# Kernel optimization log

Hardware: AMD Instinct MI355X
Metric: run time of the kernel (lower is better)

## Reference

```python
import jax, jax.numpy as jnp
import numpy as np

B, L, D, H, FF, V, NL = 1024, 200, 128, 4, 512, 100001, 2
DK = D // H
EPS = 1e-5


def layer_norm(x, w, b):
    mu = jnp.mean(x, axis=-1, keepdims=True)
    var = jnp.mean(jnp.square(x - mu), axis=-1, keepdims=True)
    return (x - mu) * jax.lax.rsqrt(var + EPS) * w + b


def setup_inputs() -> dict:
    key = jax.random.key(0)
    ks = jax.random.split(key, 32)
    s = 0.02
    d = {}
    d["batch_seqs"] = jax.random.randint(ks[0], (B, L), 0, V, dtype=jnp.int32)
    d["token_emb"] = jax.random.normal(ks[1], (V, D), jnp.float32) * s
    d["pos_emb"] = jax.random.normal(ks[2], (L, D), jnp.float32) * s
    # per-layer stacked params, leading axis = layer
    d["Wq"] = jax.random.normal(ks[3], (NL, D, D), jnp.float32) * s
    d["bq"] = jnp.zeros((NL, D), jnp.float32)
    d["Wk"] = jax.random.normal(ks[4], (NL, D, D), jnp.float32) * s
    d["bk"] = jnp.zeros((NL, D), jnp.float32)
    d["Wv"] = jax.random.normal(ks[5], (NL, D, D), jnp.float32) * s
    d["bv"] = jnp.zeros((NL, D), jnp.float32)
    d["Wo"] = jax.random.normal(ks[6], (NL, D, D), jnp.float32) * s
    d["bo"] = jnp.zeros((NL, D), jnp.float32)
    d["ln1_w"] = jnp.ones((NL, D), jnp.float32)
    d["ln1_b"] = jnp.zeros((NL, D), jnp.float32)
    d["ln2_w"] = jnp.ones((NL, D), jnp.float32)
    d["ln2_b"] = jnp.zeros((NL, D), jnp.float32)
    d["W1"] = jax.random.normal(ks[7], (NL, D, FF), jnp.float32) * s
    d["b1"] = jnp.zeros((NL, FF), jnp.float32)
    d["W2"] = jax.random.normal(ks[8], (NL, FF, D), jnp.float32) * s
    d["b2"] = jnp.zeros((NL, D), jnp.float32)
    d["fc_W"] = jax.random.normal(ks[9], (L * D, D), jnp.float32) * s
    d["fc_b"] = jnp.zeros((D,), jnp.float32)
    return d


def reference(batch_seqs, token_emb, pos_emb, Wq, bq, Wk, bk, Wv, bv, Wo, bo,
              ln1_w, ln1_b, ln2_w, ln2_b, W1, b1, W2, b2, fc_W, fc_b):
    # key-padding mask: [B,1,1,L] (broadcasts over heads and queries)
    mask = (batch_seqs > 0)[:, None, None, :]
    x = token_emb[batch_seqs] + pos_emb[None, :, :]  # [B,L,D]
    scale = 1.0 / jnp.sqrt(jnp.float32(DK))
    for i in range(NL):
        h = layer_norm(x, ln1_w[i], ln1_b[i])
        q = (h @ Wq[i] + bq[i]).reshape(B, L, H, DK)
        k = (h @ Wk[i] + bk[i]).reshape(B, L, H, DK)
        v = (h @ Wv[i] + bv[i]).reshape(B, L, H, DK)
        scores = jnp.einsum('bqhd,bkhd->bhqk', q, k) * scale
        scores = jnp.where(mask, scores, -1e9)
        p = jax.nn.softmax(scores, axis=-1)
        attn = jnp.einsum('bhqk,bkhd->bqhd', p, v).reshape(B, L, D)
        x = x + (attn @ Wo[i] + bo[i])
        h = layer_norm(x, ln2_w[i], ln2_b[i])
        ffn = jax.nn.gelu(h @ W1[i] + b1[i], approximate=False) @ W2[i] + b2[i]
        x = x + ffn
    # FlattenLayers: flatten [B, L*D] -> Linear -> [B, D]
    out = x.reshape(B, L * D) @ fc_W + fc_b
    return out
```

## Files before the change

### kernel.cpp

```cpp
#include <hip/hip_runtime.h>
#include <math.h>

typedef unsigned short u16;
typedef unsigned int u32;
typedef __attribute__((ext_vector_type(8))) short bf16x8;
typedef __attribute__((ext_vector_type(4))) float f32x4;

#define Bx 1024
#define Lx 200
#define Dx 128
#define FFx 512
#define Mx (Bx*Lx)
#define PVP 232
#define TSP 40

__device__ __forceinline__ u16 f2bf(float f) {
  u32 u = __float_as_uint(f);
  u32 r = (u + 0x7fffu + ((u >> 16) & 1u)) >> 16;
  return (u16)r;
}

__device__ __forceinline__ float gelu_f(float v) {
  float z = v * fmaf(v * v, 0.0713548163f, 1.5957691216f);
  float e = __expf(-z);
  return v * __builtin_amdgcn_rcpf(1.0f + e);
}

union BFCV { u32 u[4]; bf16x8 h; };

struct CvtJobs {
  const float* src[13];
  u16* dst[13];
  int N[13];
  int ks[13];
  int bstart[14];
};

__global__ void k_cvt_all(CvtJobs J) {
  const int b = blockIdx.x;
  int j = 0;
  #pragma unroll 1
  while (b >= J.bstart[j + 1]) ++j;
  const float* __restrict__ src = J.src[j];
  u16* __restrict__ dst = J.dst[j];
  const int N = J.N[j], k_steps = J.ks[j];
  int id = (b - J.bstart[j]) * 256 + threadIdx.x;
  int lane = id & 63;
  int rest = id >> 6;
  int kst = rest % k_steps;
  int ntile = rest / k_steps;
  int n = ntile * 16 + (lane & 15);
  int kb = kst * 32 + ((lane >> 4) << 3);
  const float* sp = src + (size_t)kb * N + n;
  u32 w[4];
  #pragma unroll
  for (int jj = 0; jj < 4; ++jj) {
    u32 lo = f2bf(sp[(size_t)(2 * jj) * N]);
    u32 hi = f2bf(sp[(size_t)(2 * jj + 1) * N]);
    w[jj] = lo | (hi << 16);
  }
  ((uint4*)dst)[id] = make_uint4(w[0], w[1], w[2], w[3]);
}

__global__ void k_embed(const int* __restrict__ seq, const float* __restrict__ tok,
                        const float* __restrict__ pos, float* __restrict__ x) {
  const int i = blockIdx.x * 256 + threadIdx.x;
  const int row = i >> 5, c = i & 31;
  const int t = seq[row];
  const int l = row % Lx;
  const float4 a = ((const float4*)tok)[(size_t)t * 32 + c];
  const float4 p = ((const float4*)pos)[l * 32 + c];
  ((float4*)x)[i] = make_float4(a.x + p.x, a.y + p.y, a.z + p.z, a.w + p.w);
}

__device__ __forceinline__ void reg_ln(const float* __restrict__ xr,
                                       const float* __restrict__ ln_w,
                                       const float* __restrict__ ln_b,
                                       int quad, bf16x8 af[4]) {
  float v[32];
  float s = 0.f, sq = 0.f;
  #pragma unroll
  for (int kst = 0; kst < 4; ++kst) {
    float4 a = *(const float4*)(xr + kst * 32);
    float4 b = *(const float4*)(xr + kst * 32 + 4);
    v[kst * 8 + 0] = a.x; v[kst * 8 + 1] = a.y; v[kst * 8 + 2] = a.z; v[kst * 8 + 3] = a.w;
    v[kst * 8 + 4] = b.x; v[kst * 8 + 5] = b.y; v[kst * 8 + 6] = b.z; v[kst * 8 + 7] = b.w;
  }
  #pragma unroll
  for (int i = 0; i < 32; ++i) { s += v[i]; sq = fmaf(v[i], v[i], sq); }
  s  += __shfl_xor(s, 16);  s  += __shfl_xor(s, 32);
  sq += __shfl_xor(sq, 16); sq += __shfl_xor(sq, 32);
  float mu = s * 0.0078125f;
  float rr = rsqrtf(fmaf(-mu, mu, sq * 0.0078125f) + 1e-5f);
  #pragma unroll
  for (int kst = 0; kst < 4; ++kst) {
    const float* lwp = ln_w + kst * 32 + quad * 8;
    const float* lbp = ln_b + kst * 32 + quad * 8;
    float4 lw0 = *(const float4*)(lwp);
    float4 lw1 = *(const float4*)(lwp + 4);
    float4 lb0 = *(const float4*)(lbp);
    float4 lb1 = *(const float4*)(lbp + 4);
    float hw[8] = {lw0.x, lw0.y, lw0.z, lw0.w, lw1.x, lw1.y, lw1.z, lw1.w};
    float hb[8] = {lb0.x, lb0.y, lb0.z, lb0.w, lb1.x, lb1.y, lb1.z, lb1.w};
    BFCV cv;
    #pragma unroll
    for (int j = 0; j < 4; ++j) {
      float h0 = fmaf((v[kst * 8 + 2 * j]     - mu) * rr, hw[2 * j],     hb[2 * j]);
      float h1 = fmaf((v[kst * 8 + 2 * j + 1] - mu) * rr, hw[2 * j + 1], hb[2 * j + 1]);
      cv.u[j] = (u32)f2bf(h0) | ((u32)f2bf(h1) << 16);
    }
    af[kst] = cv.h;
  }
}

__global__ __launch_bounds__(256, 4)
void k_qkv(const float* __restrict__ x, const float* __restrict__ ln_w,
           const float* __restrict__ ln_b, const u16* __restrict__ Wqkvs,
           const float* __restrict__ bq, const float* __restrict__ bk,
           const float* __restrict__ bv,
           u16* __restrict__ qo, u16* __restrict__ ko, u16* __restrict__ vo) {
  const int tid = threadIdx.x;
  const int row0 = blockIdx.x * 64;
  const int lane = tid & 63, wv = tid >> 6;
  const int l15 = lane & 15, quad = lane >> 4;
  const int m0 = wv * 16;

  bf16x8 af[4];
  reg_ln(x + (size_t)(row0 + m0 + l15) * Dx + quad * 8, ln_w, ln_b, quad, af);

  int bl[4], ll[4];
  #pragma unroll
  for (int r = 0; r < 4; ++r) {
    int gr = row0 + m0 + quad * 4 + r;
    bl[r] = gr / 200;
    ll[r] = gr - bl[r] * 200;
  }

  const float scale = 0.17677669529663687f;
  #pragma unroll
  for (int nt = 0; nt < 24; ++nt) {
    f32x4 acc = (f32x4){0.f, 0.f, 0.f, 0.f};
    const u16* wb = Wqkvs + ((size_t)(nt * 4) * 64 + lane) * 8;
    #pragma unroll
    for (int kst = 0; kst < 4; ++kst) {
      bf16x8 bfr = *(const bf16x8*)(wb + kst * 64 * 8);
      acc = __builtin_amdgcn_mfma_f32_16x16x32_bf16(af[kst], bfr, acc, 0, 0, 0);
    }
    const int col = (nt & 7) * 16 + l15;
    const int head = col >> 5, dk = col & 31;
    if (nt < 8) {
      float bb = bq[col];
      #pragma unroll
      for (int r = 0; r < 4; ++r)
        qo[((size_t)(bl[r] * 4 + head) * 200 + ll[r]) * 32 + dk] = f2bf((acc[r] + bb) * scale);
    } else if (nt < 16) {
      float bb = bk[col];
      #pragma unroll
      for (int r = 0; r < 4; ++r)
        ko[((size_t)(bl[r] * 4 + head) * 200 + ll[r]) * 32 + dk] = f2bf(acc[r] + bb);
    } else {
      float bb = bv[col];
      #pragma unroll
      for (int r = 0; r < 4; ++r)
        vo[((size_t)(bl[r] * 4 + head) * 200 + ll[r]) * 32 + dk] = f2bf(acc[r] + bb);
    }
  }
}

__global__ __launch_bounds__(256, 3)
void k_attn2(const u16* __restrict__ q, const u16* __restrict__ k,
             const u16* __restrict__ v, const int* __restrict__ seq,
             u16* __restrict__ attn) {
  __shared__ float smask[224];
  __shared__ __align__(16) u16 vt[32 * PVP];
  __shared__ __align__(16) u16 Pb[4][16 * PVP];
  const int tid = threadIdx.x;
  const int bl = blockIdx.x >> 2, head = blockIdx.x & 3;
  const int bh = blockIdx.x;
  const int lane = tid & 63, wv = tid >> 6;
  const int l15 = lane & 15, quad = lane >> 4;

  if (tid < 224)
    smask[tid] = (tid < 200 && seq[bl * 200 + tid] > 0) ? 0.f : -1e9f;
  #pragma unroll 1
  for (int e = tid; e < 800; e += 256) {
    int l = e >> 2, g = (e & 3) * 8;
    uint4 pv = *(const uint4*)(v + ((size_t)bh * 200 + l) * 32 + g);
    const u16* pw = (const u16*)&pv;
    #pragma unroll
    for (int j = 0; j < 8; ++j) vt[(g + j) * PVP + l] = pw[j];
  }
  #pragma unroll 1
  for (int e = tid; e < 1024; e += 256) {
    int rr = e >> 5, cc = 200 + (e & 31);
    vt[rr * PVP + cc] = 0;
  }
  __syncthreads();

  float msk[14];
  #pragma unroll
  for (int nt = 0; nt < 14; ++nt) msk[nt] = smask[nt * 16 + l15];

  const u16* qbase = q + (size_t)bh * 200 * 32;
  const u16* kbase = k + (size_t)bh * 200 * 32;
  u16* Pw = Pb[wv];

  #pragma unroll 1
  for (int mt = wv; mt < 13; mt += 4) {
    bf16x8 qf = *(const bf16x8*)(qbase + (mt * 16 + l15) * 32 + quad * 8);
    f32x4 s[14];
    #pragma unroll
    for (int nt = 0; nt < 14; ++nt) {
      bf16x8 kf = *(const bf16x8*)(kbase + (nt * 16 + l15) * 32 + quad * 8);
      s[nt] = __builtin_amdgcn_mfma_f32_16x16x32_bf16(qf, kf, (f32x4){0.f, 0.f, 0.f, 0.f}, 0, 0, 0);
    }
    float rmax[4] = {-1e30f, -1e30f, -1e30f, -1e30f};
    #pragma unroll
    for (int nt = 0; nt < 14; ++nt) {
      #pragma unroll
      for (int r = 0; r < 4; ++r) {
        s[nt][r] += msk[nt];
        rmax[r] = fmaxf(rmax[r], s[nt][r]);
      }
    }
    #pragma unroll
    for (int m = 1; m < 16; m <<= 1) {
      #pragma unroll
      for (int r = 0; r < 4; ++r) rmax[r] = fmaxf(rmax[r], __shfl_xor(rmax[r], m));
    }
    float rsum[4] = {0.f, 0.f, 0.f, 0.f};
    #pragma unroll
    for (int nt = 0; nt < 14; ++nt) {
      #pragma unroll
      for (int r = 0; r < 4; ++r) {
        float p = __expf(s[nt][r] - rmax[r]);
        s[nt][r] = p;
        rsum[r] += p;
      }
    }
    #pragma unroll
    for (int m = 1; m < 16; m <<= 1) {
      #pragma unroll
      for (int r = 0; r < 4; ++r) rsum[r] += __shfl_xor(rsum[r], m);
    }
    float inv[4];
    #pragma unroll
    for (int r = 0; r < 4; ++r) inv[r] = 1.0f / rsum[r];
    #pragma unroll
    for (int nt = 0; nt < 14; ++nt) {
      #pragma unroll
      for (int r = 0; r < 4; ++r)
        Pw[(quad * 4 + r) * PVP + nt * 16 + l15] = f2bf(s[nt][r]);
    }
    __asm__ __volatile__("s_waitcnt lgkmcnt(0)" ::: "memory");
    f32x4 o0 = (f32x4){0.f, 0.f, 0.f, 0.f}, o1 = (f32x4){0.f, 0.f, 0.f, 0.f};
    #pragma unroll
    for (int kst = 0; kst < 7; ++kst) {
      bf16x8 pf  = *(const bf16x8*)&Pw[l15 * PVP + kst * 32 + quad * 8];
      bf16x8 vf0 = *(const bf16x8*)&vt[l15 * PVP + kst * 32 + quad * 8];
      bf16x8 vf1 = *(const bf16x8*)&vt[(16 + l15) * PVP + kst * 32 + quad * 8];
      o0 = __builtin_amdgcn_mfma_f32_16x16x32_bf16(pf, vf0, o0, 0, 0, 0);
      o1 = __builtin_amdgcn_mfma_f32_16x16x32_bf16(pf, vf1, o1, 0, 0, 0);
    }
    #pragma unroll
    for (int r = 0; r < 4; ++r) {
      int row = mt * 16 + quad * 4 + r;
      if (row < 200) {
        u16* op = attn + ((size_t)bl * 200 + row) * 128 + head * 32;
        op[l15]      = f2bf(o0[r] * inv[r]);
        op[16 + l15] = f2bf(o1[r] * inv[r]);
      }
    }
  }
}

__global__ __launch_bounds__(256, 4)
void k_oproj(const u16* __restrict__ a, const u16* __restrict__ Wos,
             const float* __restrict__ bo, float* __restrict__ x) {
  const int tid = threadIdx.x;
  const int lane = tid & 63, wv = tid >> 6;
  const int l15 = lane & 15, quad = lane >> 4;
  const size_t m0 = (size_t)blockIdx.x * 64 + wv * 16;
  f32x4 acc[8];
  #pragma unroll
  for (int i = 0; i < 8; ++i) acc[i] = (f32x4){0.f, 0.f, 0.f, 0.f};
  #pragma unroll
  for (int kst = 0; kst < 4; ++kst) {
    bf16x8 af = *(const bf16x8*)(a + (m0 + l15) * Dx + kst * 32 + quad * 8);
    const u16* wb = Wos + (kst * 64 + lane) * 8;
    #pragma unroll
    for (int nt = 0; nt < 8; ++nt) {
      bf16x8 bf = *(const bf16x8*)(wb + nt * (4 * 64 * 8));
      acc[nt] = __builtin_amdgcn_mfma_f32_16x16x32_bf16(af, bf, acc[nt], 0, 0, 0);
    }
  }
  #pragma unroll
  for (int nt = 0; nt < 8; ++nt) {
    int col = nt * 16 + l15;
    float bb = bo[col];
    #pragma unroll
    for (int r = 0; r < 4; ++r) {
      size_t idx = (m0 + quad * 4 + r) * Dx + col;
      x[idx] += acc[nt][r] + bb;
    }
  }
}

__global__ __launch_bounds__(256, 4)
void k_ffn(float* __restrict__ x, const float* __restrict__ ln_w,
           const float* __restrict__ ln_b,
           const u16* __restrict__ W1s, const float* __restrict__ b1,
           const u16* __restrict__ W2s, const float* __restrict__ b2) {
  __shared__ __align__(16) u16 smem[2560 + 8192 + 8192];
  u16* ts  = smem;
  u16* w1b = smem + 2560;
  u16* w2b = smem + 10752;
  const int tid = threadIdx.x;
  const size_t row0 = (size_t)blockIdx.x * 64;
  const int lane = tid & 63, wv = tid >> 6;
  const int l15 = lane & 15, quad = lane >> 4;
  const int m0 = wv * 16;
  const int nt0 = tid >> 6, off = tid & 63;

  bf16x8 af[4];
  reg_ln(x + (row0 + m0 + l15) * (size_t)Dx + quad * 8, ln_w, ln_b, quad, af);

  ((uint4*)w1b)[tid]       = ((const uint4*)(W1s + (size_t)(nt0 * 4) * 512))[off];
  ((uint4*)w1b)[tid + 256] = ((const uint4*)(W1s + (size_t)((nt0 + 4) * 4) * 512))[off];
  ((uint4*)w2b)[tid]       = ((const uint4*)(W2s + (size_t)(nt0 * 16) * 512))[off];
  ((uint4*)w2b)[tid + 256] = ((const uint4*)(W2s + (size_t)((nt0 + 4) * 16) * 512))[off];
  __syncthreads();

  f32x4 acc2[8];
  #pragma unroll
  for (int i = 0; i < 8; ++i) acc2[i] = (f32x4){0.f, 0.f, 0.f, 0.f};

  #pragma unroll 1
  for (int ch = 0; ch < 4; ++ch) {
    f32x4 acc1[8];
    #pragma unroll
    for (int i = 0; i < 8; ++i) acc1[i] = (f32x4){0.f, 0.f, 0.f, 0.f};
    #pragma unroll
    for (int kst = 0; kst < 4; ++kst) {
      uint4 s0, s1;
      if (kst < 3) {
        s0 = ((const uint4*)(W1s + (size_t)((ch * 8 + nt0) * 4 + kst + 1) * 512))[off];
        s1 = ((const uint4*)(W1s + (size_t)((ch * 8 + nt0 + 4) * 4 + kst + 1) * 512))[off];
      }
      const u16* wb = w1b + (kst & 1) * 4096;
      #pragma unroll
      for (int nt = 0; nt < 8; ++nt) {
        bf16x8 bfr = *(const bf16x8*)&wb[nt * 512 + lane * 8];
        acc1[nt] = __builtin_amdgcn_mfma_f32_16x16x32_bf16(af[kst], bfr, acc1[nt], 0, 0, 0);
      }
      if (kst < 3) {
        uint4* d = (uint4*)(w1b + ((kst + 1) & 1) * 4096);
        d[tid] = s0; d[tid + 256] = s1;
      }
      __syncthreads();
    }
    #pragma unroll
    for (int p = 0; p < 4; ++p) {
      uint4 s0, s1, t0, t1;
      const bool s2  = (p < 3);
      const bool s1n = (p == 3) && (ch < 3);
      if (s2) {
        s0 = ((const uint4*)(W2s + (size_t)(nt0 * 16 + ch * 4 + p + 1) * 512))[off];
        s1 = ((const uint4*)(W2s + (size_t)((nt0 + 4) * 16 + ch * 4 + p + 1) * 512))[off];
      }
      if (s1n) {
        s0 = ((const uint4*)(W1s + (size_t)(((ch + 1) * 8 + nt0) * 4) * 512))[off];
        s1 = ((const uint4*)(W1s + (size_t)(((ch + 1) * 8 + nt0 + 4) * 4) * 512))[off];
        t0 = ((const uint4*)(W2s + (size_t)(nt0 * 16 + (ch + 1) * 4) * 512))[off];
        t1 = ((const uint4*)(W2s + (size_t)((nt0 + 4) * 16 + (ch + 1) * 4) * 512))[off];
      }
      #pragma unroll
      for (int q2 = 0; q2 < 2; ++q2) {
        const int ntg = 2 * p + q2;
        float bb = b1[ch * 128 + ntg * 16 + l15];
        #pragma unroll
        for (int r = 0; r < 4; ++r)
          ts[(m0 + quad * 4 + r) * TSP + q2 * 16 + l15] =
              f2bf(gelu_f(acc1[ntg][r] + bb));
      }
      __asm__ __volatile__("s_waitcnt lgkmcnt(0)" ::: "memory");
      bf16x8 tf = *(const bf16x8*)&ts[(m0 + l15) * TSP + quad * 8];
      const u16* wb = w2b + (p & 1) * 4096;
      #pragma unroll
      for (int nt = 0; nt < 8; ++nt) {
        bf16x8 bfr = *(const bf16x8*)&wb[nt * 512 + lane * 8];
        acc2[nt] = __builtin_amdgcn_mfma_f32_16x16x32_bf16(tf, bfr, acc2[nt], 0, 0, 0);
      }
      if (s2) {
        uint4* d = (uint4*)(w2b + ((p + 1) & 1) * 4096);
        d[tid] = s0; d[tid + 256] = s1;
      }
      if (s1n) {
        ((uint4*)w1b)[tid] = s0; ((uint4*)w1b)[tid + 256] = s1;
        ((uint4*)w2b)[tid] = t0; ((uint4*)w2b)[tid + 256] = t1;
      }
      __syncthreads();
    }
  }
  #pragma unroll
  for (int nt = 0; nt < 8; ++nt) {
    int col = nt * 16 + l15;
    float bb = b2[col];
    #pragma unroll
    for (int r = 0; r < 4; ++r) {
      size_t idx = (row0 + m0 + quad * 4 + r) * Dx + col;
      x[idx] += acc2[nt][r] + bb;
    }
  }
}

__global__ __launch_bounds__(256, 4)
void k_fc(const float* __restrict__ x, const u16* __restrict__ fcWs,
          float* __restrict__ part) {
  const int tid = threadIdx.x;
  const int lane = tid & 63, wv = tid >> 6;
  const int l15 = lane & 15, quad = lane >> 4;
  const int m0 = blockIdx.x * 64 + wv * 16;
  const int ky = blockIdx.y;
  f32x4 acc[8];
  #pragma unroll
  for (int i = 0; i < 8; ++i) acc[i] = (f32x4){0.f, 0.f, 0.f, 0.f};
  const float* xp = x + (size_t)(m0 + l15) * 25600 + quad * 8;
  #pragma unroll 1
  for (int kst = ky * 25; kst < ky * 25 + 25; ++kst) {
    float4 xa = *(const float4*)(xp + kst * 32);
    float4 xb2 = *(const float4*)(xp + kst * 32 + 4);
    bf16x8 af;
    af[0] = (short)f2bf(xa.x);  af[1] = (short)f2bf(xa.y);
    af[2] = (short)f2bf(xa.z);  af[3] = (short)f2bf(xa.w);
    af[4] = (short)f2bf(xb2.x); af[5] = (short)f2bf(xb2.y);
    af[6] = (short)f2bf(xb2.z); af[7] = (short)f2bf(xb2.w);
    const u16* wb = fcWs + ((size_t)kst * 64 + lane) * 8;
    #pragma unroll
    for (int nt = 0; nt < 8; ++nt) {
      bf16x8 bf = *(const bf16x8*)(wb + (size_t)nt * (800 * 64 * 8));
      acc[nt] = __builtin_amdgcn_mfma_f32_16x16x32_bf16(af, bf, acc[nt], 0, 0, 0);
    }
  }
  float* pp = part + (size_t)ky * (Bx * Dx);
  #pragma unroll
  for (int nt = 0; nt < 8; ++nt) {
    #pragma unroll
    for (int r = 0; r < 4; ++r) {
      pp[(size_t)(m0 + quad * 4 + r) * Dx + nt * 16 + l15] = acc[nt][r];
    }
  }
}

__global__ void k_fcred(const float* __restrict__ part, const float* __restrict__ fcb,
                        float* __restrict__ out) {
  int i = blockIdx.x * 256 + threadIdx.x;
  float s = fcb[i & 127];
  #pragma unroll
  for (int k = 0; k < 32; ++k) s += part[(size_t)k * (Bx * Dx) + i];
  out[i] = s;
}

extern "C" void kernel_launch(void* const* d_in, const int* in_sizes, int n_in,
                              void* d_out, int out_size, void* d_ws, size_t ws_size,
                              hipStream_t stream) {
  const int*   seq  = (const int*)d_in[0];
  const float* tok  = (const float*)d_in[1];
  const float* pos  = (const float*)d_in[2];
  const float* Wq   = (const float*)d_in[3];
  const float* bq   = (const float*)d_in[4];
  const float* Wk   = (const float*)d_in[5];
  const float* bk   = (const float*)d_in[6];
  const float* Wv   = (const float*)d_in[7];
  const float* bv   = (const float*)d_in[8];
  const float* Wo   = (const float*)d_in[9];
  const float* bo   = (const float*)d_in[10];
  const float* ln1w = (const float*)d_in[11];
  const float* ln1b = (const float*)d_in[12];
  const float* ln2w = (const float*)d_in[13];
  const float* ln2b = (const float*)d_in[14];
  const float* W1   = (const float*)d_in[15];
  const float* b1   = (const float*)d_in[16];
  const float* W2   = (const float*)d_in[17];
  const float* b2   = (const float*)d_in[18];
  const float* fcW  = (const float*)d_in[19];
  const float* fcb  = (const float*)d_in[20];
  float* out = (float*)d_out;

  char* ws = (char*)d_ws;
  const size_t XB = (size_t)Mx * Dx * 4;
  const size_t WBSZ = 7340032;

  int nc = 4;
  for (int t = 1; t <= 4; t <<= 1) {
    size_t qsz = (size_t)(Bx / t) * 51200;
    if (XB + 4 * qsz + WBSZ <= ws_size) { nc = t; break; }
  }
  const int BC = Bx / nc;
  const size_t qsz = (size_t)BC * 51200;

  float* x    = (float*)ws;
  u16* qb     = (u16*)(ws + XB);
  u16* kb     = (u16*)(ws + XB + qsz);
  u16* vb     = (u16*)(ws + XB + 2 * qsz);
  u16* ab     = (u16*)(ws + XB + 3 * qsz);
  float* part = (float*)(ws + XB);
  char* WB    = ws + XB + 4 * qsz;
  u16* W1s0   = (u16*)(WB);
  u16* W1s1   = (u16*)(WB + 131072);
  u16* W2s0   = (u16*)(WB + 262144);
  u16* W2s1   = (u16*)(WB + 393216);
  u16* Wos0   = (u16*)(WB + 524288);
  u16* Wos1   = (u16*)(WB + 557056);
  u16* Wqkvs0 = (u16*)(WB + 589824);
  u16* Wqkvs1 = (u16*)(WB + 688128);
  u16* fcWs   = (u16*)(WB + 786432);

  CvtJobs J;
  const float* srcs[13] = {W1, W1 + Dx * FFx, W2, W2 + FFx * Dx,
                           Wo, Wo + Dx * Dx,
                           Wq, Wk, Wv,
                           Wq + Dx * Dx, Wk + Dx * Dx, Wv + Dx * Dx,
                           fcW};
  u16* dsts[13] = {W1s0, W1s1, W2s0, W2s1, Wos0, Wos1,
                   Wqkvs0, Wqkvs0 + 16384, Wqkvs0 + 32768,
                   Wqkvs1, Wqkvs1 + 16384, Wqkvs1 + 32768,
                   fcWs};
  const int Ns[13]  = {FFx, FFx, Dx, Dx, Dx, Dx, Dx, Dx, Dx, Dx, Dx, Dx, Dx};
  const int kss[13] = {4, 4, 16, 16, 4, 4, 4, 4, 4, 4, 4, 4, 800};
  const int nblk[13] = {32, 32, 32, 32, 8, 8, 8, 8, 8, 8, 8, 8, 1600};
  int acc = 0;
  for (int j = 0; j < 13; ++j) {
    J.src[j] = srcs[j]; J.dst[j] = dsts[j]; J.N[j] = Ns[j]; J.ks[j] = kss[j];
    J.bstart[j] = acc; acc += nblk[j];
  }
  J.bstart[13] = acc;
  k_cvt_all<<<acc, 256, 0, stream>>>(J);

  k_embed<<<25600, 256, 0, stream>>>(seq, tok, pos, x);
  const int cblk = BC * 200 / 64;
  for (int i = 0; i < 2; ++i) {
    const u16* Wqkvs = (i == 0) ? Wqkvs0 : Wqkvs1;
    const u16* Wos   = (i == 0) ? Wos0 : Wos1;
    for (int c = 0; c < nc; ++c) {
      float* xc = x + (size_t)c * BC * 200 * 128;
      const int* seqc = seq + (size_t)c * BC * 200;
      k_qkv<<<cblk, 256, 0, stream>>>(xc, ln1w + i * Dx, ln1b + i * Dx, Wqkvs,
                                      bq + i * Dx, bk + i * Dx, bv + i * Dx,
                                      qb, kb, vb);
      k_attn2<<<BC * 4, 256, 0, stream>>>(qb, kb, vb, seqc, ab);
      k_oproj<<<cblk, 256, 0, stream>>>(ab, Wos, bo + i * Dx, xc);
    }
    k_ffn<<<3200, 256, 0, stream>>>(x, ln2w + i * Dx, ln2b + i * Dx,
                                    (i == 0) ? W1s0 : W1s1, b1 + i * FFx,
                                    (i == 0) ? W2s0 : W2s1, b2 + i * Dx);
  }
  k_fc<<<dim3(16, 32), 256, 0, stream>>>(x, fcWs, part);
  k_fcred<<<512, 256, 0, stream>>>(part, fcb, out);
}
```

Before: 919.0 us.

## Process two 16-row tiles per wave in QKV and FFN kernels

Each wave in k_qkv and k_ffn now computes two 16-row M tiles, so every loaded weight fragment feeds two MFMAs. The QKV kernel handles 128 rows per block, halving its grid. The FFN kernel drops to 128 threads and replaces its separate W1 and W2 double buffers with one shared ping-pong buffer, cutting LDS use. In exchange, accumulator register pressure doubles and there are fewer waves per block, which may reduce occupancy and latency hiding.

Result: slower. 2.044 ms (+122.4%).

```diff
diff --git a/kernel.cpp b/kernel.cpp
--- a/kernel.cpp
+++ b/kernel.cpp
@@ -120,49 +120,62 @@
            const float* __restrict__ bv,
            u16* __restrict__ qo, u16* __restrict__ ko, u16* __restrict__ vo) {
   const int tid = threadIdx.x;
-  const int row0 = blockIdx.x * 64;
+  const int row0 = blockIdx.x * 128;
   const int lane = tid & 63, wv = tid >> 6;
   const int l15 = lane & 15, quad = lane >> 4;
-  const int m0 = wv * 16;
-
-  bf16x8 af[4];
-  reg_ln(x + (size_t)(row0 + m0 + l15) * Dx + quad * 8, ln_w, ln_b, quad, af);
-
-  int bl[4], ll[4];
-  #pragma unroll
-  for (int r = 0; r < 4; ++r) {
-    int gr = row0 + m0 + quad * 4 + r;
-    bl[r] = gr / 200;
-    ll[r] = gr - bl[r] * 200;
-  }
+  const int m0 = wv * 32;
+
+  bf16x8 af[2][4];
+  #pragma unroll
+  for (int rt = 0; rt < 2; ++rt)
+    reg_ln(x + (size_t)(row0 + m0 + rt * 16 + l15) * Dx + quad * 8,
+           ln_w, ln_b, quad, af[rt]);
+
+  int bl[2][4], ll[2][4];
+  #pragma unroll
+  for (int rt = 0; rt < 2; ++rt)
+    #pragma unroll
+    for (int r = 0; r < 4; ++r) {
+      int gr = row0 + m0 + rt * 16 + quad * 4 + r;
+      bl[rt][r] = gr / 200;
+      ll[rt][r] = gr - bl[rt][r] * 200;
+    }
 
   const float scale = 0.17677669529663687f;
   #pragma unroll
   for (int nt = 0; nt < 24; ++nt) {
-    f32x4 acc = (f32x4){0.f, 0.f, 0.f, 0.f};
+    f32x4 a0 = (f32x4){0.f, 0.f, 0.f, 0.f};
+    f32x4 a1 = (f32x4){0.f, 0.f, 0.f, 0.f};
     const u16* wb = Wqkvs + ((size_t)(nt * 4) * 64 + lane) * 8;
     #pragma unroll
     for (int kst = 0; kst < 4; ++kst) {
       bf16x8 bfr = *(const bf16x8*)(wb + kst * 64 * 8);
-      acc = __builtin_amdgcn_mfma_f32_16x16x32_bf16(af[kst], bfr, acc, 0, 0, 0);
+      a0 = __builtin_amdgcn_mfma_f32_16x16x32_bf16(af[0][kst], bfr, a0, 0, 0, 0);
+      a1 = __builtin_amdgcn_mfma_f32_16x16x32_bf16(af[1][kst], bfr, a1, 0, 0, 0);
     }
     const int col = (nt & 7) * 16 + l15;
     const int head = col >> 5, dk = col & 31;
     if (nt < 8) {
       float bb = bq[col];
       #pragma unroll
-      for (int r = 0; r < 4; ++r)
-        qo[((size_t)(bl[r] * 4 + head) * 200 + ll[r]) * 32 + dk] = f2bf((acc[r] + bb) * scale);
+      for (int r = 0; r < 4; ++r) {
+        qo[((size_t)(bl[0][r] * 4 + head) * 200 + ll[0][r]) * 32 + dk] = f2bf((a0[r] + bb) * scale);
+        qo[((size_t)(bl[1][r] * 4 + head) * 200 + ll[1][r]) * 32 + dk] = f2bf((a1[r] + bb) * scale);
+      }
     } else if (nt < 16) {
       float bb = bk[col];
       #pragma unroll
-      for (int r = 0; r < 4; ++r)
-        ko[((size_t)(bl[r] * 4 + head) * 200 + ll[r]) * 32 + dk] = f2bf(acc[r] + bb);
+      for (int r = 0; r < 4; ++r) {
+        ko[((size_t)(bl[0][r] * 4 + head) * 200 + ll[0][r]) * 32 + dk] = f2bf(a0[r] + bb);
+        ko[((size_t)(bl[1][r] * 4 + head) * 200 + ll[1][r]) * 32 + dk] = f2bf(a1[r] + bb);
+      }
     } else {
       float bb = bv[col];
       #pragma unroll
-      for (int r = 0; r < 4; ++r)
-        vo[((size_t)(bl[r] * 4 + head) * 200 + ll[r]) * 32 + dk] = f2bf(acc[r] + bb);
+      for (int r = 0; r < 4; ++r) {
+        vo[((size_t)(bl[0][r] * 4 + head) * 200 + ll[0][r]) * 32 + dk] = f2bf(a0[r] + bb);
+        vo[((size_t)(bl[1][r] * 4 + head) * 200 + ll[1][r]) * 32 + dk] = f2bf(a1[r] + bb);
+      }
     }
   }
 }
@@ -306,112 +319,134 @@
   }
 }
 
-__global__ __launch_bounds__(256, 4)
+__global__ __launch_bounds__(128, 4)
 void k_ffn(float* __restrict__ x, const float* __restrict__ ln_w,
            const float* __restrict__ ln_b,
            const u16* __restrict__ W1s, const float* __restrict__ b1,
            const u16* __restrict__ W2s, const float* __restrict__ b2) {
-  __shared__ __align__(16) u16 smem[2560 + 8192 + 8192];
-  u16* ts  = smem;
-  u16* w1b = smem + 2560;
-  u16* w2b = smem + 10752;
+  __shared__ __align__(16) u16 smem[2560 + 2 * 4096];
+  u16* ts   = smem;
+  u16* wbuf = smem + 2560;
   const int tid = threadIdx.x;
   const size_t row0 = (size_t)blockIdx.x * 64;
   const int lane = tid & 63, wv = tid >> 6;
   const int l15 = lane & 15, quad = lane >> 4;
-  const int m0 = wv * 16;
-  const int nt0 = tid >> 6, off = tid & 63;
-
-  bf16x8 af[4];
-  reg_ln(x + (row0 + m0 + l15) * (size_t)Dx + quad * 8, ln_w, ln_b, quad, af);
-
-  ((uint4*)w1b)[tid]       = ((const uint4*)(W1s + (size_t)(nt0 * 4) * 512))[off];
-  ((uint4*)w1b)[tid + 256] = ((const uint4*)(W1s + (size_t)((nt0 + 4) * 4) * 512))[off];
-  ((uint4*)w2b)[tid]       = ((const uint4*)(W2s + (size_t)(nt0 * 16) * 512))[off];
-  ((uint4*)w2b)[tid + 256] = ((const uint4*)(W2s + (size_t)((nt0 + 4) * 16) * 512))[off];
+  const int m0 = wv * 32;
+
+  bf16x8 af[2][4];
+  #pragma unroll
+  for (int rt = 0; rt < 2; ++rt)
+    reg_ln(x + (row0 + m0 + rt * 16 + l15) * (size_t)Dx + quad * 8,
+           ln_w, ln_b, quad, af[rt]);
+
+  int snt[4], sof[4];
+  #pragma unroll
+  for (int i = 0; i < 4; ++i) { int e = tid + i * 128; snt[i] = e >> 6; sof[i] = e & 63; }
+
+  #pragma unroll
+  for (int i = 0; i < 4; ++i)
+    ((uint4*)wbuf)[tid + i * 128] =
+        ((const uint4*)(W1s + (size_t)(snt[i] * 4) * 512))[sof[i]];
   __syncthreads();
 
-  f32x4 acc2[8];
-  #pragma unroll
-  for (int i = 0; i < 8; ++i) acc2[i] = (f32x4){0.f, 0.f, 0.f, 0.f};
-
+  f32x4 acc2[2][8];
+  #pragma unroll
+  for (int rt = 0; rt < 2; ++rt)
+    #pragma unroll
+    for (int i = 0; i < 8; ++i) acc2[rt][i] = (f32x4){0.f, 0.f, 0.f, 0.f};
+
+  int pq = 0;
   #pragma unroll 1
   for (int ch = 0; ch < 4; ++ch) {
-    f32x4 acc1[8];
-    #pragma unroll
-    for (int i = 0; i < 8; ++i) acc1[i] = (f32x4){0.f, 0.f, 0.f, 0.f};
+    f32x4 acc1[2][8];
+    #pragma unroll
+    for (int rt = 0; rt < 2; ++rt)
+      #pragma unroll
+      for (int i = 0; i < 8; ++i) acc1[rt][i] = (f32x4){0.f, 0.f, 0.f, 0.f};
     #pragma unroll
     for (int kst = 0; kst < 4; ++kst) {
-      uint4 s0, s1;
+      uint4 sg[4];
       if (kst < 3) {
-        s0 = ((const uint4*)(W1s + (size_t)((ch * 8 + nt0) * 4 + kst + 1) * 512))[off];
-        s1 = ((const uint4*)(W1s + (size_t)((ch * 8 + nt0 + 4) * 4 + kst + 1) * 512))[off];
-      }
-      const u16* wb = w1b + (kst & 1) * 4096;
+        #pragma unroll
+        for (int i = 0; i < 4; ++i)
+          sg[i] = ((const uint4*)(W1s + (size_t)((ch * 8 + snt[i]) * 4 + kst + 1) * 512))[sof[i]];
+      } else {
+        #pragma unroll
+        for (int i = 0; i < 4; ++i)
+          sg[i] = ((const uint4*)(W2s + (size_t)(snt[i] * 16 + ch * 4) * 512))[sof[i]];
+      }
+      const u16* wb = wbuf + pq * 4096;
       #pragma unroll
       for (int nt = 0; nt < 8; ++nt) {
         bf16x8 bfr = *(const bf16x8*)&wb[nt * 512 + lane * 8];
-        acc1[nt] = __builtin_amdgcn_mfma_f32_16x16x32_bf16(af[kst], bfr, acc1[nt], 0, 0, 0);
-      }
-      if (kst < 3) {
-        uint4* d = (uint4*)(w1b + ((kst + 1) & 1) * 4096);
-        d[tid] = s0; d[tid + 256] = s1;
+        acc1[0][nt] = __builtin_amdgcn_mfma_f32_16x16x32_bf16(af[0][kst], bfr, acc1[0][nt], 0, 0, 0);
+        acc1[1][nt] = __builtin_amdgcn_mfma_f32_16x16x32_bf16(af[1][kst], bfr, acc1[1][nt], 0, 0, 0);
+      }
+      {
+        uint4* d = (uint4*)(wbuf + (pq ^ 1) * 4096);
+        #pragma unroll
+        for (int i = 0; i < 4; ++i) d[tid + i * 128] = sg[i];
       }
       __syncthreads();
+      pq ^= 1;
     }
     #pragma unroll
     for (int p = 0; p < 4; ++p) {
-      uint4 s0, s1, t0, t1;
-      const bool s2  = (p < 3);
-      const bool s1n = (p == 3) && (ch < 3);
-      if (s2) {
-        s0 = ((const uint4*)(W2s + (size_t)(nt0 * 16 + ch * 4 + p + 1) * 512))[off];
-        s1 = ((const uint4*)(W2s + (size_t)((nt0 + 4) * 16 + ch * 4 + p + 1) * 512))[off];
-      }
-      if (s1n) {
-        s0 = ((const uint4*)(W1s + (size_t)(((ch + 1) * 8 + nt0) * 4) * 512))[off];
-        s1 = ((const uint4*)(W1s + (size_t)(((ch + 1) * 8 + nt0 + 4) * 4) * 512))[off];
-        t0 = ((const uint4*)(W2s + (size_t)(nt0 * 16 + (ch + 1) * 4) * 512))[off];
-        t1 = ((const uint4*)(W2s + (size_t)((nt0 + 4) * 16 + (ch + 1) * 4) * 512))[off];
-      }
-      #pragma unroll
-      for (int q2 = 0; q2 < 2; ++q2) {
-        const int ntg = 2 * p + q2;
-        float bb = b1[ch * 128 + ntg * 16 + l15];
-        #pragma unroll
-        for (int r = 0; r < 4; ++r)
-          ts[(m0 + quad * 4 + r) * TSP + q2 * 16 + l15] =
-              f2bf(gelu_f(acc1[ntg][r] + bb));
-      }
+      uint4 sg[4];
+      bool have = true;
+      if (p < 3) {
+        #pragma unroll
+        for (int i = 0; i < 4; ++i)
+          sg[i] = ((const uint4*)(W2s + (size_t)(snt[i] * 16 + ch * 4 + p + 1) * 512))[sof[i]];
+      } else if (ch < 3) {
+        #pragma unroll
+        for (int i = 0; i < 4; ++i)
+          sg[i] = ((const uint4*)(W1s + (size_t)(((ch + 1) * 8 + snt[i]) * 4) * 512))[sof[i]];
+      } else {
+        have = false;
+      }
+      #pragma unroll
+      for (int rt = 0; rt < 2; ++rt)
+        #pragma unroll
+        for (int q2 = 0; q2 < 2; ++q2) {
+          const int ntg = 2 * p + q2;
+          float bb = b1[ch * 128 + ntg * 16 + l15];
+          #pragma unroll
+          for (int r = 0; r < 4; ++r)
+            ts[(m0 + rt * 16 + quad * 4 + r) * TSP + q2 * 16 + l15] =
+                f2bf(gelu_f(acc1[rt][ntg][r] + bb));
+        }
       __asm__ __volatile__("s_waitcnt lgkmcnt(0)" ::: "memory");
-      bf16x8 tf = *(const bf16x8*)&ts[(m0 + l15) * TSP + quad * 8];
-      const u16* wb = w2b + (p & 1) * 4096;
+      bf16x8 tf0 = *(const bf16x8*)&ts[(m0 + l15) * TSP + quad * 8];
+      bf16x8 tf1 = *(const bf16x8*)&ts[(m0 + 16 + l15) * TSP + quad * 8];
+      const u16* wb = wbuf + pq * 4096;
       #pragma unroll
       for (int nt = 0; nt < 8; ++nt) {
         bf16x8 bfr = *(const bf16x8*)&wb[nt * 512 + lane * 8];
-        acc2[nt] = __builtin_amdgcn_mfma_f32_16x16x32_bf16(tf, bfr, acc2[nt], 0, 0, 0);
-      }
-      if (s2) {
-        uint4* d = (uint4*)(w2b + ((p + 1) & 1) * 4096);
-        d[tid] = s0; d[tid + 256] = s1;
-      }
-      if (s1n) {
-        ((uint4*)w1b)[tid] = s0; ((uint4*)w1b)[tid + 256] = s1;
-        ((uint4*)w2b)[tid] = t0; ((uint4*)w2b)[tid + 256] = t1;
+        acc2[0][nt] = __builtin_amdgcn_mfma_f32_16x16x32_bf16(tf0, bfr, acc2[0][nt], 0, 0, 0);
+        acc2[1][nt] = __builtin_amdgcn_mfma_f32_16x16x32_bf16(tf1, bfr, acc2[1][nt], 0, 0, 0);
+      }
+      if (have) {
+        uint4* d = (uint4*)(wbuf + (pq ^ 1) * 4096);
+        #pragma unroll
+        for (int i = 0; i < 4; ++i) d[tid + i * 128] = sg[i];
       }
       __syncthreads();
-    }
-  }
-  #pragma unroll
-  for (int nt = 0; nt < 8; ++nt) {
-    int col = nt * 16 + l15;
-    float bb = b2[col];
-    #pragma unroll
-    for (int r = 0; r < 4; ++r) {
-      size_t idx = (row0 + m0 + quad * 4 + r) * Dx + col;
-      x[idx] += acc2[nt][r] + bb;
-    }
-  }
+      pq ^= 1;
+    }
+  }
+  #pragma unroll
+  for (int rt = 0; rt < 2; ++rt)
+    #pragma unroll
+    for (int nt = 0; nt < 8; ++nt) {
+      int col = nt * 16 + l15;
+      float bb = b2[col];
+      #pragma unroll
+      for (int r = 0; r < 4; ++r) {
+        size_t idx = (row0 + m0 + rt * 16 + quad * 4 + r) * Dx + col;
+        x[idx] += acc2[rt][nt][r] + bb;
+      }
+    }
 }
 
 __global__ __launch_bounds__(256, 4)
@@ -538,7 +573,8 @@
   k_cvt_all<<<acc, 256, 0, stream>>>(J);
 
   k_embed<<<25600, 256, 0, stream>>>(seq, tok, pos, x);
-  const int cblk = BC * 200 / 64;
+  const int cblk = BC * 200 / 128;
+  const int oblk = BC * 200 / 64;
   for (int i = 0; i < 2; ++i) {
     const u16* Wqkvs = (i == 0) ? Wqkvs0 : Wqkvs1;
     const u16* Wos   = (i == 0) ? Wos0 : Wos1;
@@ -549,9 +585,9 @@
                                       bq + i * Dx, bk + i * Dx, bv + i * Dx,
                                       qb, kb, vb);
       k_attn2<<<BC * 4, 256, 0, stream>>>(qb, kb, vb, seqc, ab);
-      k_oproj<<<cblk, 256, 0, stream>>>(ab, Wos, bo + i * Dx, xc);
-    }
-    k_ffn<<<3200, 256, 0, stream>>>(x, ln2w + i * Dx, ln2b + i * Dx,
+      k_oproj<<<oblk, 256, 0, stream>>>(ab, Wos, bo + i * Dx, xc);
+    }
+    k_ffn<<<3200, 128, 0, stream>>>(x, ln2w + i * Dx, ln2b + i * Dx,
                                     (i == 0) ? W1s0 : W1s1, b1 + i * FFx,
                                     (i == 0) ? W2s0 : W2s1, b2 + i * Dx);
   }
```

## Fuse output projection and residual add into FFN kernel

Applied to the files above, without the earlier changes.

The attention output projection (Wo GEMM plus residual add) moves into the FFN kernel, which now reads the bf16 attention output for the whole batch. A full-size attention buffer is allocated when the workspace is large enough, and the chunk count is recomputed to fit it. This removes one kernel launch per chunk and one write/read round trip of x between oproj and the FFN's layernorm. In exchange the FFN kernel carries more work and register pressure, and it needs a larger workspace, which may force more chunks for the QKV and attention passes.

Result: slower. 1.033 ms (+12.4%).

```diff
diff --git a/kernel.cpp b/kernel.cpp
--- a/kernel.cpp
+++ b/kernel.cpp
@@ -307,8 +307,9 @@
 }
 
 __global__ __launch_bounds__(256, 4)
-void k_ffn(float* __restrict__ x, const float* __restrict__ ln_w,
-           const float* __restrict__ ln_b,
+void k_ffn(float* __restrict__ x, const u16* __restrict__ abp,
+           const u16* __restrict__ Wos, const float* __restrict__ bo,
+           const float* __restrict__ ln_w, const float* __restrict__ ln_b,
            const u16* __restrict__ W1s, const float* __restrict__ b1,
            const u16* __restrict__ W2s, const float* __restrict__ b2) {
   __shared__ __align__(16) u16 smem[2560 + 8192 + 8192];
@@ -322,8 +323,34 @@
   const int m0 = wv * 16;
   const int nt0 = tid >> 6, off = tid & 63;
 
-  bf16x8 af[4];
-  reg_ln(x + (row0 + m0 + l15) * (size_t)Dx + quad * 8, ln_w, ln_b, quad, af);
+  f32x4 acc2[8];
+  #pragma unroll
+  for (int i = 0; i < 8; ++i) acc2[i] = (f32x4){0.f, 0.f, 0.f, 0.f};
+
+  if (abp) {
+    #pragma unroll
+    for (int kst = 0; kst < 4; ++kst) {
+      bf16x8 abf = *(const bf16x8*)(abp + (row0 + m0 + l15) * (size_t)Dx + kst * 32 + quad * 8);
+      const u16* wb = Wos + (kst * 64 + lane) * 8;
+      #pragma unroll
+      for (int nt = 0; nt < 8; ++nt) {
+        bf16x8 wf = *(const bf16x8*)(wb + nt * (4 * 64 * 8));
+        acc2[nt] = __builtin_amdgcn_mfma_f32_16x16x32_bf16(abf, wf, acc2[nt], 0, 0, 0);
+      }
+    }
+    #pragma unroll
+    for (int nt = 0; nt < 8; ++nt) {
+      int col = nt * 16 + l15;
+      float bb = bo[col];
+      #pragma unroll
+      for (int r = 0; r < 4; ++r) {
+        size_t idx = (row0 + m0 + quad * 4 + r) * Dx + col;
+        float xn = x[idx] + acc2[nt][r] + bb;
+        acc2[nt][r] = xn;
+        x[idx] = xn;
+      }
+    }
+  }
 
   ((uint4*)w1b)[tid]       = ((const uint4*)(W1s + (size_t)(nt0 * 4) * 512))[off];
   ((uint4*)w1b)[tid + 256] = ((const uint4*)(W1s + (size_t)((nt0 + 4) * 4) * 512))[off];
@@ -331,9 +358,8 @@
   ((uint4*)w2b)[tid + 256] = ((const uint4*)(W2s + (size_t)((nt0 + 4) * 16) * 512))[off];
   __syncthreads();
 
-  f32x4 acc2[8];
-  #pragma unroll
-  for (int i = 0; i < 8; ++i) acc2[i] = (f32x4){0.f, 0.f, 0.f, 0.f};
+  bf16x8 af[4];
+  reg_ln(x + (row0 + m0 + l15) * (size_t)Dx + quad * 8, ln_w, ln_b, quad, af);
 
   #pragma unroll 1
   for (int ch = 0; ch < 4; ++ch) {
@@ -409,7 +435,8 @@
     #pragma unroll
     for (int r = 0; r < 4; ++r) {
       size_t idx = (row0 + m0 + quad * 4 + r) * Dx + col;
-      x[idx] += acc2[nt][r] + bb;
+      if (abp) x[idx] = acc2[nt][r] + bb;
+      else     x[idx] += acc2[nt][r] + bb;
     }
   }
 }
@@ -488,14 +515,17 @@
   float* out = (float*)d_out;
 
   char* ws = (char*)d_ws;
-  const size_t XB = (size_t)Mx * Dx * 4;
+  const size_t XB  = (size_t)Mx * Dx * 4;
+  const size_t ABF = (size_t)Mx * Dx * 2;
   const size_t WBSZ = 7340032;
 
-  int nc = 4;
-  for (int t = 1; t <= 4; t <<= 1) {
-    size_t qsz = (size_t)(Bx / t) * 51200;
-    if (XB + 4 * qsz + WBSZ <= ws_size) { nc = t; break; }
-  }
+  int nc = 0;
+  for (int t = 1; t <= 32; t <<= 1) {
+    size_t q3 = 3 * ((size_t)(Bx / t) * 51200);
+    if (XB + q3 + ABF + WBSZ <= ws_size) { nc = t; break; }
+  }
+  const bool fused = (nc != 0);
+  if (!fused) nc = 4;
   const int BC = Bx / nc;
   const size_t qsz = (size_t)BC * 51200;
 
@@ -505,7 +535,7 @@
   u16* vb     = (u16*)(ws + XB + 2 * qsz);
   u16* ab     = (u16*)(ws + XB + 3 * qsz);
   float* part = (float*)(ws + XB);
-  char* WB    = ws + XB + 4 * qsz;
+  char* WB    = fused ? (ws + XB + 3 * qsz + ABF) : (ws + XB + 4 * qsz);
   u16* W1s0   = (u16*)(WB);
   u16* W1s1   = (u16*)(WB + 131072);
   u16* W2s0   = (u16*)(WB + 262144);
@@ -548,10 +578,13 @@
       k_qkv<<<cblk, 256, 0, stream>>>(xc, ln1w + i * Dx, ln1b + i * Dx, Wqkvs,
                                       bq + i * Dx, bk + i * Dx, bv + i * Dx,
                                       qb, kb, vb);
-      k_attn2<<<BC * 4, 256, 0, stream>>>(qb, kb, vb, seqc, ab);
-      k_oproj<<<cblk, 256, 0, stream>>>(ab, Wos, bo + i * Dx, xc);
-    }
-    k_ffn<<<3200, 256, 0, stream>>>(x, ln2w + i * Dx, ln2b + i * Dx,
+      u16* abc = fused ? ab + (size_t)c * BC * 200 * 128 : ab;
+      k_attn2<<<BC * 4, 256, 0, stream>>>(qb, kb, vb, seqc, abc);
+      if (!fused)
+        k_oproj<<<cblk, 256, 0, stream>>>(ab, Wos, bo + i * Dx, xc);
+    }
+    k_ffn<<<3200, 256, 0, stream>>>(x, fused ? ab : nullptr, Wos, bo + i * Dx,
+                                    ln2w + i * Dx, ln2b + i * Dx,
                                     (i == 0) ? W1s0 : W1s1, b1 + i * FFx,
                                     (i == 0) ? W2s0 : W2s1, b2 + i * Dx);
   }
```
